# Kernel optimization log

Measured on AMD Instinct MI355X. Metric: run time of the kernel, lower is better.

Reference implementation:

```python
import jax, jax.numpy as jnp
import numpy as np

INF = 1e10  # sentinel 'infinity' for non-feature pixels (safe to add (s*N)^2 without overflow)


def _edt_sq_last(f, s):
    """Exact 1D squared distance transform along the last axis.
    f: (..., N) initialized to 0 at feature pixels, INF elsewhere.
    Returns g[..., i] = min_j f[..., j] + (s*(i-j))^2.
    Sequential lax.scan over output positions keeps memory at O(N) extra."""
    N = f.shape[-1]
    j = jnp.arange(N, dtype=f.dtype)

    def step(_, i):
        return None, jnp.min(f + (s * (i - j)) ** 2, axis=-1)

    _, out = jax.lax.scan(step, None, jnp.arange(N, dtype=f.dtype))
    return jnp.moveaxis(out, 0, -1)


def _edt(feature_mask, sampling):
    """Euclidean distance to the nearest True pixel of feature_mask (2D, anisotropic sampling).
    Equivalent to scipy.ndimage.distance_transform_edt(~feature_mask, sampling=sampling)."""
    f = jnp.where(feature_mask, 0.0, INF).astype(jnp.float32)
    # pass over axis -2 (rows), then axis -1 (cols) -- exact separable squared EDT
    f = jnp.moveaxis(_edt_sq_last(jnp.moveaxis(f, -2, -1), sampling[0]), -1, -2)
    f = _edt_sq_last(f, sampling[1])
    return jnp.sqrt(f)


def _distance_map(y_onehot, sampling):
    """res = edt_to_pos * negmask - (edt_to_neg - 1) * posmask, 0 where class absent."""
    pos = y_onehot              # (B,K,H,W) bool
    neg = ~pos
    d_neg = _edt(pos, sampling)  # distance of neg pixels to nearest pos pixel
    d_pos = _edt(neg, sampling)  # distance of pos pixels to nearest neg pixel
    res = jnp.where(neg, d_neg, 0.0) - jnp.where(pos, d_pos - 1.0, 0.0)
    has_pos = pos.any(axis=(-2, -1), keepdims=True)  # scipy path leaves res[k]=0 if class absent
    return jnp.where(has_pos, res, 0.0)


def reference(x, y):
    # x: (B,K,H,W) float; y: (B,1,H,W) int labels in [0,K)
    K = x.shape[1]
    y_onehot = (y == jnp.arange(K, dtype=y.dtype)[None, :, None, None])  # scatter_ onehot
    dist_map = jax.lax.stop_gradient(_distance_map(y_onehot, (1.0, 1.0)))
    return jnp.mean(x * dist_map)  # einsum('bkwh,bkwh->bkwh').mean()


def setup_inputs() -> dict:
    key = jax.random.key(0)
    k1, k2 = jax.random.split(key)
    x = jax.random.normal(k1, (8, 4, 256, 256), dtype=jnp.float32)
    y = jax.random.randint(k2, (8, 1, 256, 256), 0, 4, dtype=jnp.int32)
    return {"x": x, "y": y}
```

## Files before the change

kernel.cpp:

```cpp
#include <hip/hip_runtime.h>


#define HH 256
#define WW 256
#define NPIX (HH*WW)
#define NPM 64
#define NBLK2 1024
#define ROWS_PER_BLK 16
#define BIG (1 << 27)

#define SEGS 8
#define RSEG 32
#define CPB 32

__global__ void edt_vpass(const int* __restrict__ y, unsigned short* __restrict__ g) {
    __shared__ unsigned short d[HH][CPB + 1];
    __shared__ short segLast[SEGS][CPB];
    __shared__ short segFirst[SEGS][CPB];

    int bid   = blockIdx.x;
    int pm    = bid >> 3;
    int cc    = bid & 7;
    int which = pm & 1;
    int plane = pm >> 1;
    int b     = plane >> 2;
    int k     = plane & 3;

    int t   = threadIdx.x;
    int col = t & (CPB - 1);
    int seg = t >> 5;
    int w   = cc * CPB + col;
    int h0  = seg * RSEG;

    const int* yp = y + b * NPIX;
    unsigned short* gp = g + (size_t)pm * NPIX;

    int lastL = -1000, firstL = 1000;
    for (int i = 0; i < RSEG; ++i) {
        int h   = h0 + i;
        int lab = yp[h * WW + w];
        int feat = ((lab == k) ? 1 : 0) ^ which;
        if (feat) { lastL = h; if (firstL > 900) firstL = h; }
        d[h][col] = (unsigned short)min(h - lastL, 1000);
    }
    segLast[seg][col]  = (short)lastL;
    segFirst[seg][col] = (short)firstL;
    __syncthreads();

    int prevLast = -1000;
    for (int s = seg - 1; s >= 0; --s) {
        int v = segLast[s][col];
        if (v >= 0) { prevLast = v; break; }
    }
    int nextFirst = 1000;
    for (int s = seg + 1; s < SEGS; ++s) {
        int v = segFirst[s][col];
        if (v < 900) { nextFirst = v; break; }
    }

    int nd = nextFirst;
    for (int i = RSEG - 1; i >= 0; --i) {
        int h  = h0 + i;
        int du = d[h][col];
        if (du == 0) nd = h;
        int dup = min(du, h - prevLast);
        int ddn = nd - h;
        int m   = min(min(dup, ddn), 256);
        gp[h * WW + w] = (m > 255) ? (unsigned short)0xFFFF
                                   : (unsigned short)(m * m);
    }
}

__global__ void edt_hpass(const unsigned short* __restrict__ g,
                          const float* __restrict__ x,
                          double* __restrict__ bsums) {
    __shared__ int tile[ROWS_PER_BLK][WW];
    __shared__ double wsum[4];

    int bid   = blockIdx.x;
    int pm    = bid >> 4;
    int rc    = bid & 15;
    int r0    = rc * ROWS_PER_BLK;
    int which = pm & 1;
    int plane = pm >> 1;
    int t     = threadIdx.x;

    const unsigned short* gp = g + (size_t)pm * NPIX;
    const float* xp = x + (size_t)plane * NPIX;

    const unsigned int* gp32 = (const unsigned int*)(gp + r0 * WW);
    for (int i2 = 0; i2 < 8; ++i2) {
        int idx = i2 * 256 + t;
        int row = idx >> 7;
        int c2  = idx & 127;
        unsigned int v = gp32[row * 128 + c2];
        int v0 = (int)(v & 0xFFFFu);
        int v1 = (int)(v >> 16);
        tile[row][2 * c2]     = (v0 == 0xFFFF) ? BIG : v0;
        tile[row][2 * c2 + 1] = (v1 == 0xFFFF) ? BIG : v1;
    }
    __syncthreads();

    double lsum = 0.0;
    for (int i = 0; i < ROWS_PER_BLK; ++i) {
        int best = tile[i][t];
        #pragma unroll 1
        for (int bs = 1; bs < WW; bs += 4) {
            if (bs * bs >= best) break;
            int m = best;
            #pragma unroll
            for (int u = 0; u < 4; ++u) {
                int r  = bs + u;
                int rr = r * r;
                int jl = max(t - r, 0);
                int jr = min(t + r, WW - 1);
                m = min(m, tile[i][jl] + rr);
                m = min(m, tile[i][jr] + rr);
            }
            best = m;
        }
        if (best > 0 && best < BIG) {
            float xv   = xp[(r0 + i) * WW + t];
            float dd   = sqrtf((float)best);
            float term = which ? (1.0f - dd) : dd;
            lsum += (double)(xv * term);
        }
    }

    for (int off = 32; off > 0; off >>= 1)
        lsum += __shfl_down(lsum, off, 64);
    int lane = t & 63, wv = t >> 6;
    if (lane == 0) wsum[wv] = lsum;
    __syncthreads();
    if (t == 0) bsums[bid] = wsum[0] + wsum[1] + wsum[2] + wsum[3];
}

__global__ void edt_finalize(const double* __restrict__ bsums, float* __restrict__ out) {
    __shared__ double wsum[4];
    int t = threadIdx.x;
    double s = 0.0;
    for (int i = t; i < NBLK2; i += 256) s += bsums[i];
    for (int off = 32; off > 0; off >>= 1)
        s += __shfl_down(s, off, 64);
    int lane = t & 63, wv = t >> 6;
    if (lane == 0) wsum[wv] = s;
    __syncthreads();
    if (t == 0)
        out[0] = (float)((wsum[0] + wsum[1] + wsum[2] + wsum[3]) * (1.0 / 2097152.0));
}

extern "C" void kernel_launch(void* const* d_in, const int* in_sizes, int n_in,
                              void* d_out, int out_size, void* d_ws, size_t ws_size,
                              hipStream_t stream) {
    const float* x = (const float*)d_in[0];
    const int*   y = (const int*)d_in[1];
    float* out = (float*)d_out;

    unsigned short* g = (unsigned short*)d_ws;
    double* bsums = (double*)((char*)d_ws + (size_t)NPM * NPIX * sizeof(unsigned short));

    edt_vpass   <<<512,   256, 0, stream>>>(y, g);
    edt_hpass   <<<NBLK2, 256, 0, stream>>>(g, x, bsums);
    edt_finalize<<<1,     256, 0, stream>>>(bsums, out);
}
```

Measured before the change: 78.89 us.

## Fuse vertical and horizontal EDT passes and reduction into one kernel

Merges the vertical pass, horizontal pass and final reduction into a single kernel, with one 1024-thread block per plane/mask that keeps the whole 256x256 distance plane in shared memory. The intermediate global buffer and two extra launches go away, and the cross-block sum uses a double atomic plus a ticket counter, after a memset, so the last block writes the output. In exchange the grid shrinks to 64 blocks on a GPU with many more compute units, each thread handles 64 rows serially, and the horizontal pass now reads 16-bit shared values and converts the sentinel on every access.

Result: slower. 121.1 us (+53.5%).

```diff
diff --git a/kernel.cpp b/kernel.cpp
--- a/kernel.cpp
+++ b/kernel.cpp
@@ -5,105 +5,76 @@
 #define WW 256
 #define NPIX (HH*WW)
 #define NPM 64
-#define NBLK2 1024
-#define ROWS_PER_BLK 16
 #define BIG (1 << 27)
+#define SEGS 4
+#define RSEG 64
 
-#define SEGS 8
-#define RSEG 32
-#define CPB 32
+__global__ __launch_bounds__(1024, 1) void boundary_fused(
+        const int* __restrict__ y, const float* __restrict__ x,
+        double* __restrict__ acc, unsigned int* __restrict__ cnt,
+        float* __restrict__ out)
+{
+    __shared__ unsigned short d[HH][WW];
+    __shared__ short segLast[SEGS][WW];
+    __shared__ short segFirst[SEGS][WW];
+    __shared__ double wsum[16];
+    __shared__ int lastFlag;
 
-__global__ void edt_vpass(const int* __restrict__ y, unsigned short* __restrict__ g) {
-    __shared__ unsigned short d[HH][CPB + 1];
-    __shared__ short segLast[SEGS][CPB];
-    __shared__ short segFirst[SEGS][CPB];
-
-    int bid   = blockIdx.x;
-    int pm    = bid >> 3;
-    int cc    = bid & 7;
+    int pm    = blockIdx.x;
     int which = pm & 1;
     int plane = pm >> 1;
     int b     = plane >> 2;
     int k     = plane & 3;
 
     int t   = threadIdx.x;
-    int col = t & (CPB - 1);
-    int seg = t >> 5;
-    int w   = cc * CPB + col;
+    int w   = t & (WW - 1);
+    int seg = t >> 8;
     int h0  = seg * RSEG;
 
-    const int* yp = y + b * NPIX;
-    unsigned short* gp = g + (size_t)pm * NPIX;
+    const int*   yp = y + b * NPIX;
+    const float* xp = x + (size_t)plane * NPIX;
 
     int lastL = -1000, firstL = 1000;
     for (int i = 0; i < RSEG; ++i) {
-        int h   = h0 + i;
-        int lab = yp[h * WW + w];
+        int h    = h0 + i;
+        int lab  = yp[h * WW + w];
         int feat = ((lab == k) ? 1 : 0) ^ which;
         if (feat) { lastL = h; if (firstL > 900) firstL = h; }
-        d[h][col] = (unsigned short)min(h - lastL, 1000);
+        d[h][w] = (unsigned short)min(h - lastL, 1000);
     }
-    segLast[seg][col]  = (short)lastL;
-    segFirst[seg][col] = (short)firstL;
+    segLast[seg][w]  = (short)lastL;
+    segFirst[seg][w] = (short)firstL;
     __syncthreads();
 
     int prevLast = -1000;
     for (int s = seg - 1; s >= 0; --s) {
-        int v = segLast[s][col];
+        int v = segLast[s][w];
         if (v >= 0) { prevLast = v; break; }
     }
     int nextFirst = 1000;
     for (int s = seg + 1; s < SEGS; ++s) {
-        int v = segFirst[s][col];
+        int v = segFirst[s][w];
         if (v < 900) { nextFirst = v; break; }
     }
 
     int nd = nextFirst;
     for (int i = RSEG - 1; i >= 0; --i) {
         int h  = h0 + i;
-        int du = d[h][col];
+        int du = d[h][w];
         if (du == 0) nd = h;
         int dup = min(du, h - prevLast);
         int ddn = nd - h;
         int m   = min(min(dup, ddn), 256);
-        gp[h * WW + w] = (m > 255) ? (unsigned short)0xFFFF
-                                   : (unsigned short)(m * m);
-    }
-}
-
-__global__ void edt_hpass(const unsigned short* __restrict__ g,
-                          const float* __restrict__ x,
-                          double* __restrict__ bsums) {
-    __shared__ int tile[ROWS_PER_BLK][WW];
-    __shared__ double wsum[4];
-
-    int bid   = blockIdx.x;
-    int pm    = bid >> 4;
-    int rc    = bid & 15;
-    int r0    = rc * ROWS_PER_BLK;
-    int which = pm & 1;
-    int plane = pm >> 1;
-    int t     = threadIdx.x;
-
-    const unsigned short* gp = g + (size_t)pm * NPIX;
-    const float* xp = x + (size_t)plane * NPIX;
-
-    const unsigned int* gp32 = (const unsigned int*)(gp + r0 * WW);
-    for (int i2 = 0; i2 < 8; ++i2) {
-        int idx = i2 * 256 + t;
-        int row = idx >> 7;
-        int c2  = idx & 127;
-        unsigned int v = gp32[row * 128 + c2];
-        int v0 = (int)(v & 0xFFFFu);
-        int v1 = (int)(v >> 16);
-        tile[row][2 * c2]     = (v0 == 0xFFFF) ? BIG : v0;
-        tile[row][2 * c2 + 1] = (v1 == 0xFFFF) ? BIG : v1;
+        d[h][w] = (m > 255) ? (unsigned short)0xFFFF
+                            : (unsigned short)(m * m);
     }
     __syncthreads();
 
     double lsum = 0.0;
-    for (int i = 0; i < ROWS_PER_BLK; ++i) {
-        int best = tile[i][t];
+    for (int i = 0; i < RSEG; ++i) {
+        int h  = h0 + i;
+        int gc = d[h][w];
+        int best = (gc == 0xFFFF) ? BIG : gc;
         #pragma unroll 1
         for (int bs = 1; bs < WW; bs += 4) {
             if (bs * bs >= best) break;
@@ -112,15 +83,17 @@
             for (int u = 0; u < 4; ++u) {
                 int r  = bs + u;
                 int rr = r * r;
-                int jl = max(t - r, 0);
-                int jr = min(t + r, WW - 1);
-                m = min(m, tile[i][jl] + rr);
-                m = min(m, tile[i][jr] + rr);
+                int jl = max(w - r, 0);
+                int jr = min(w + r, WW - 1);
+                int gl = d[h][jl]; gl = (gl == 0xFFFF) ? BIG : gl;
+                int gr = d[h][jr]; gr = (gr == 0xFFFF) ? BIG : gr;
+                m = min(m, gl + rr);
+                m = min(m, gr + rr);
             }
             best = m;
         }
         if (best > 0 && best < BIG) {
-            float xv   = xp[(r0 + i) * WW + t];
+            float xv   = xp[h * WW + w];
             float dd   = sqrtf((float)best);
             float term = which ? (1.0f - dd) : dd;
             lsum += (double)(xv * term);
@@ -132,21 +105,23 @@
     int lane = t & 63, wv = t >> 6;
     if (lane == 0) wsum[wv] = lsum;
     __syncthreads();
-    if (t == 0) bsums[bid] = wsum[0] + wsum[1] + wsum[2] + wsum[3];
-}
 
-__global__ void edt_finalize(const double* __restrict__ bsums, float* __restrict__ out) {
-    __shared__ double wsum[4];
-    int t = threadIdx.x;
-    double s = 0.0;
-    for (int i = t; i < NBLK2; i += 256) s += bsums[i];
-    for (int off = 32; off > 0; off >>= 1)
-        s += __shfl_down(s, off, 64);
-    int lane = t & 63, wv = t >> 6;
-    if (lane == 0) wsum[wv] = s;
+    if (t == 0) {
+        double s = 0.0;
+        #pragma unroll
+        for (int i = 0; i < 16; ++i) s += wsum[i];
+        atomicAdd(acc, s);
+        __threadfence();
+        unsigned int ticket = atomicAdd(cnt, 1u);
+        lastFlag = (ticket == NPM - 1) ? 1 : 0;
+    }
     __syncthreads();
-    if (t == 0)
-        out[0] = (float)((wsum[0] + wsum[1] + wsum[2] + wsum[3]) * (1.0 / 2097152.0));
+
+    if (lastFlag && t == 0) {
+        __threadfence();
+        double total = atomicAdd(acc, 0.0);
+        out[0] = (float)(total * (1.0 / 2097152.0));
+    }
 }
 
 extern "C" void kernel_launch(void* const* d_in, const int* in_sizes, int n_in,
@@ -156,10 +131,9 @@
     const int*   y = (const int*)d_in[1];
     float* out = (float*)d_out;
 
-    unsigned short* g = (unsigned short*)d_ws;
-    double* bsums = (double*)((char*)d_ws + (size_t)NPM * NPIX * sizeof(unsigned short));
+    double*       acc = (double*)d_ws;
+    unsigned int* cnt = (unsigned int*)((char*)d_ws + 8);
 
-    edt_vpass   <<<512,   256, 0, stream>>>(y, g);
-    edt_hpass   <<<NBLK2, 256, 0, stream>>>(g, x, bsums);
-    edt_finalize<<<1,     256, 0, stream>>>(bsums, out);
+    hipMemsetAsync(d_ws, 0, 16, stream);
+    boundary_fused<<<NPM, 1024, 0, stream>>>(y, x, acc, cnt, out);
 }
```

## Fuse finalize into hpass via atomic last-block reduction and double grid sizes

Applied to the files above, without the earlier changes.

Removes the separate finalize kernel launch by having each hpass block atomically add its partial sum into striped double accumulators, with the last block (chosen by ticket counter) reducing them and writing the output. The vertical pass now uses 16-column blocks (1024 blocks), the horizontal pass uses 8 rows per block (2048 blocks), and launch bounds are added to raise occupancy. Accumulator zeroing moves into the vpass kernel's first block. This adds atomic contention and makes the summation order nondeterministic.

Result: slower. 108.5 us (+37.5%).

```diff
diff --git a/kernel.cpp b/kernel.cpp
--- a/kernel.cpp
+++ b/kernel.cpp
@@ -5,22 +5,24 @@
 #define WW 256
 #define NPIX (HH*WW)
 #define NPM 64
-#define NBLK2 1024
-#define ROWS_PER_BLK 16
 #define BIG (1 << 27)
 
-#define SEGS 8
-#define RSEG 32
-#define CPB 32
+#define NSTRIPE 64
 
-__global__ void edt_vpass(const int* __restrict__ y, unsigned short* __restrict__ g) {
+#define SEGS 16
+#define RSEG 16
+#define CPB 16
+
+__global__ __launch_bounds__(256, 4) void edt_vpass(
+        const int* __restrict__ y, unsigned short* __restrict__ g,
+        double* __restrict__ acc, unsigned int* __restrict__ cnt) {
     __shared__ unsigned short d[HH][CPB + 1];
     __shared__ short segLast[SEGS][CPB];
     __shared__ short segFirst[SEGS][CPB];
 
     int bid   = blockIdx.x;
-    int pm    = bid >> 3;
-    int cc    = bid & 7;
+    int pm    = bid >> 4;
+    int cc    = bid & 15;
     int which = pm & 1;
     int plane = pm >> 1;
     int b     = plane >> 2;
@@ -28,9 +30,14 @@
 
     int t   = threadIdx.x;
     int col = t & (CPB - 1);
-    int seg = t >> 5;
+    int seg = t >> 4;
     int w   = cc * CPB + col;
     int h0  = seg * RSEG;
+
+    if (bid == 0) {
+        if (t < NSTRIPE * 8) acc[t] = 0.0;
+        if (t == 0) *cnt = 0u;
+    }
 
     const int* yp = y + b * NPIX;
     unsigned short* gp = g + (size_t)pm * NPIX;
@@ -71,15 +78,20 @@
     }
 }
 
-__global__ void edt_hpass(const unsigned short* __restrict__ g,
-                          const float* __restrict__ x,
-                          double* __restrict__ bsums) {
+#define ROWS_PER_BLK 8
+#define NBLK2 2048
+
+__global__ __launch_bounds__(256, 8) void edt_hpass(
+        const unsigned short* __restrict__ g, const float* __restrict__ x,
+        double* __restrict__ acc, unsigned int* __restrict__ cnt,
+        float* __restrict__ out) {
     __shared__ int tile[ROWS_PER_BLK][WW];
     __shared__ double wsum[4];
+    __shared__ int lastFlag;
 
     int bid   = blockIdx.x;
-    int pm    = bid >> 4;
-    int rc    = bid & 15;
+    int pm    = bid >> 5;
+    int rc    = bid & 31;
     int r0    = rc * ROWS_PER_BLK;
     int which = pm & 1;
     int plane = pm >> 1;
@@ -89,7 +101,8 @@
     const float* xp = x + (size_t)plane * NPIX;
 
     const unsigned int* gp32 = (const unsigned int*)(gp + r0 * WW);
-    for (int i2 = 0; i2 < 8; ++i2) {
+    #pragma unroll
+    for (int i2 = 0; i2 < 4; ++i2) {
         int idx = i2 * 256 + t;
         int row = idx >> 7;
         int c2  = idx & 127;
@@ -132,21 +145,23 @@
     int lane = t & 63, wv = t >> 6;
     if (lane == 0) wsum[wv] = lsum;
     __syncthreads();
-    if (t == 0) bsums[bid] = wsum[0] + wsum[1] + wsum[2] + wsum[3];
-}
 
-__global__ void edt_finalize(const double* __restrict__ bsums, float* __restrict__ out) {
-    __shared__ double wsum[4];
-    int t = threadIdx.x;
-    double s = 0.0;
-    for (int i = t; i < NBLK2; i += 256) s += bsums[i];
-    for (int off = 32; off > 0; off >>= 1)
-        s += __shfl_down(s, off, 64);
-    int lane = t & 63, wv = t >> 6;
-    if (lane == 0) wsum[wv] = s;
+    if (t == 0) {
+        double s = wsum[0] + wsum[1] + wsum[2] + wsum[3];
+        atomicAdd(&acc[(bid & (NSTRIPE - 1)) * 8], s);
+        __threadfence();
+        unsigned int ticket = atomicAdd(cnt, 1u);
+        lastFlag = (ticket == NBLK2 - 1) ? 1 : 0;
+    }
     __syncthreads();
-    if (t == 0)
-        out[0] = (float)((wsum[0] + wsum[1] + wsum[2] + wsum[3]) * (1.0 / 2097152.0));
+
+    if (lastFlag && t < 64) {
+        __threadfence();
+        double v = atomicAdd(&acc[t * 8], 0.0);
+        for (int off = 32; off > 0; off >>= 1)
+            v += __shfl_down(v, off, 64);
+        if (t == 0) out[0] = (float)(v * (1.0 / 2097152.0));
+    }
 }
 
 extern "C" void kernel_launch(void* const* d_in, const int* in_sizes, int n_in,
@@ -156,10 +171,10 @@
     const int*   y = (const int*)d_in[1];
     float* out = (float*)d_out;
 
-    unsigned short* g = (unsigned short*)d_ws;
-    double* bsums = (double*)((char*)d_ws + (size_t)NPM * NPIX * sizeof(unsigned short));
+    unsigned short* g   = (unsigned short*)d_ws;
+    double*         acc = (double*)((char*)d_ws + (size_t)NPM * NPIX * sizeof(unsigned short));
+    unsigned int*   cnt = (unsigned int*)((char*)acc + NSTRIPE * 8 * sizeof(double));
 
-    edt_vpass   <<<512,   256, 0, stream>>>(y, g);
-    edt_hpass   <<<NBLK2, 256, 0, stream>>>(g, x, bsums);
-    edt_finalize<<<1,     256, 0, stream>>>(bsums, out);
+    edt_vpass<<<1024, 256, 0, stream>>>(y, g, acc, cnt);
+    edt_hpass<<<NBLK2, 256, 0, stream>>>(g, x, acc, cnt, out);
 }
```
